# Kernel optimization log

Measured on AMD Instinct MI355X. Metric: run time of the kernel, lower is better.

Reference implementation:

```python
import jax, jax.numpy as jnp
import numpy as np

PF = 16      # PATCH_FEATURES
PFD = 16     # PATCH_FEATURES_DEEP
NCLS = 10

def setup_inputs() -> dict:
    key = jax.random.key(0)
    ks = jax.random.split(key, 7)
    B = 131072
    x = jax.random.normal(ks[0], (B, 1, 28, 28), dtype=jnp.float32)
    # Linear params: W stored as [out, in] like torch, scaled kaiming-uniform-ish
    W1 = jax.random.uniform(ks[1], (PF, 49), jnp.float32, -1, 1) / jnp.sqrt(49.0)
    b1 = jax.random.uniform(ks[2], (PF,), jnp.float32, -1, 1) / jnp.sqrt(49.0)
    W2 = jax.random.uniform(ks[3], (PFD, 4 * PF), jnp.float32, -1, 1) / jnp.sqrt(64.0)
    b2 = jax.random.uniform(ks[4], (PFD,), jnp.float32, -1, 1) / jnp.sqrt(64.0)
    W3 = jax.random.uniform(ks[5], (NCLS, 4 * PFD), jnp.float32, -1, 1) / jnp.sqrt(64.0)
    b3 = jax.random.uniform(ks[6], (NCLS,), jnp.float32, -1, 1) / jnp.sqrt(64.0)
    return {"x": x, "W1": W1, "b1": b1, "W2": W2, "b2": b2, "W3": W3, "b3": b3}


def reference(x, W1, b1, W2, b2, W3, b3):
    # Dropout layers are identity in eval/inference mode.
    B = x.shape[0]
    img = x[:, 0]  # [B,28,28]
    # 16 non-overlapping 7x7 patches, flattened row-major (matches the torch slices)
    p = img.reshape(B, 4, 7, 4, 7).transpose(0, 1, 3, 2, 4).reshape(B, 4, 4, 49)
    # fc1 applied to every patch: one batched GEMM instead of 16 launches
    h = jnp.einsum('bijp,fp->bijf', p, W1) + b1          # [B,4,4,16]
    # group 2x2 patch blocks; concat order (x11,x12,x21,x22) = row-major (ii,jj)
    hb = h.reshape(B, 2, 2, 2, 2, PF).transpose(0, 1, 3, 2, 4, 5).reshape(B, 2, 2, 4 * PF)
    y = jnp.einsum('bijp,fp->bijf', hb, W2) + b2         # [B,2,2,16]
    # concat (y11,y12,y21,y22) row-major over (bi,bj), relu, fc3
    yflat = jax.nn.relu(y).reshape(B, 4 * PFD)           # [B,64]
    z = yflat @ W3.T + b3                                # [B,10]
    return jax.nn.log_softmax(z, axis=1)
```

## Files before the change

### kernel.cpp

```cpp
#include <hip/hip_runtime.h>

typedef float f32x4 __attribute__((ext_vector_type(4)));
typedef short bf16x8 __attribute__((ext_vector_type(8)));

#define XS 464
#define WOFF 29696
#define YOFF 29696
#define YS 144
#define BOFF 38912

__device__ __forceinline__ unsigned short f2bf(float f) {
  unsigned u = __builtin_bit_cast(unsigned, f);
  u += 0x7FFFu + ((u >> 16) & 1u);
  return (unsigned short)(u >> 16);
}
__device__ __forceinline__ unsigned packbf2(float a, float b) {
  return (unsigned)f2bf(a) | ((unsigned)f2bf(b) << 16);
}

__global__ __launch_bounds__(256, 2) void mnist_mfma(
    const float* __restrict__ x, const float* __restrict__ W1,
    const float* __restrict__ b1, const float* __restrict__ W2,
    const float* __restrict__ b2, const float* __restrict__ W3,
    const float* __restrict__ b3, float* __restrict__ out, int nimg)
{
  __shared__ __align__(16) char smem[38976];
  float* smemF = (float*)smem;
  const int tid = threadIdx.x;
  const int lane = tid & 63;
  const int waveid = tid >> 6;

  for (int i = tid; i < 784; i += 256) smemF[i] = W1[i];
  for (int i = tid; i < 1024; i += 256) smemF[784 + i] = W2[i];
  __syncthreads();

  unsigned short* w12b = (unsigned short*)(smem + WOFF);
  for (int e = tid; e < 3136; e += 256) {
    int f2 = e / 196, k = e - f2 * 196;
    int r14 = k / 14, c14 = k - r14 * 14;
    int pp = (r14 % 7) * 7 + (c14 % 7);
    int q = (r14 / 7) * 2 + (c14 / 7);
    float s = 0.f;
#pragma unroll
    for (int f = 0; f < 16; ++f)
      s = fmaf(smemF[f * 49 + pp], smemF[784 + f2 * 64 + q * 16 + f], s);
    w12b[f2 * 232 + k] = f2bf(s);
  }
  for (int e = tid; e < 576; e += 256) {
    int f2 = e / 36;
    w12b[f2 * 232 + 196 + (e - f2 * 36)] = 0;
  }
  if (tid < 16) {
    float s = b2[tid];
#pragma unroll
    for (int k = 0; k < 64; ++k)
      s = fmaf(b1[k & 15], smemF[784 + tid * 64 + k], s);
    smemF[BOFF / 4 + tid] = s;
  }
  __syncthreads();

  bf16x8 wfrag[7];
#pragma unroll
  for (int i = 0; i < 7; ++i)
    wfrag[i] = *(const bf16x8*)(smem + WOFF + (lane & 15) * XS + (lane >> 4) * 16 + 64 * i);

  bf16x8 w3f[2];
  {
    int o = lane & 15, kb = (lane >> 4) * 8;
#pragma unroll
    for (int mi = 0; mi < 2; ++mi) {
      float v[8];
#pragma unroll
      for (int j = 0; j < 8; ++j)
        v[j] = (o < 10) ? W3[o * 64 + kb + 32 * mi + j] : 0.f;
      unsigned t[4];
      t[0] = packbf2(v[0], v[1]); t[1] = packbf2(v[2], v[3]);
      t[2] = packbf2(v[4], v[5]); t[3] = packbf2(v[6], v[7]);
      w3f[mi] = __builtin_bit_cast(bf16x8, *(unsigned(*)[4])t);
    }
  }
  const float b12v = smemF[BOFF / 4 + (lane & 15)];
  float b3v[4];
#pragma unroll
  for (int r = 0; r < 4; ++r) {
    int o = (lane >> 4) * 4 + r;
    b3v[r] = (o < 10) ? b3[o] : 0.f;
  }
  __syncthreads();

  char* xw = smem + waveid * 7424;
#pragma unroll
  for (int j = 0; j < 5; ++j) {
    int idx = lane + 64 * j;
    if (idx < 288) {
      int row = idx / 18, d = idx - row * 18;
      *(unsigned*)(xw + row * XS + 392 + d * 4) = 0;
    }
  }

  unsigned wa0[13]; unsigned strm = 0;
#pragma unroll
  for (int it = 0; it < 13; ++it) {
    int gi = lane + 64 * it;
    int im = gi / 196, rem = gi - im * 196;
    int rr = rem / 7, t = rem - rr * 7;
    int c2 = 2 * t;
    int J = c2 / 7, cq = c2 - 7 * J;
    int row = im * 4 + (rr / 14) * 2 + J;
    int kp = (rr % 14) * 7 + cq;
    wa0[it] = waveid * 7424 + row * XS + kp * 4;
    if (t == 3) strm |= (1u << it);
  }

  const unsigned xrd = waveid * 7424 + (lane & 15) * XS + (lane >> 4) * 16;
  const unsigned yw_base = YOFF + waveid * 2304 + (lane & 15) * 2;
  const unsigned yrd = YOFF + waveid * 2304 + (lane & 15) * YS + (lane >> 4) * 16;

  const int NU = nimg >> 4;
  const int WST = (int)(gridDim.x << 2);
  const int w0 = (int)(blockIdx.x << 2) + waveid;
  const int ng4 = nimg >> 2;

  f32x4 cur[13];
  const f32x4* __restrict__ xq0 = (const f32x4*)x;
  auto issue4 = [&](int g4) {
    const f32x4* p = xq0 + (size_t)g4 * 784;
#pragma unroll
    for (int it = 0; it < 12; ++it) cur[it] = p[lane + 64 * it];
    if (lane < 16) cur[12] = p[768 + lane];
  };

  if (w0 < NU) issue4(w0 * 4);

  for (int u = w0; u < NU; u += WST) {
#pragma unroll 1
    for (int sb = 0; sb < 4; ++sb) {
#pragma unroll
      for (int it = 0; it < 13; ++it) {
        if (it == 12 && lane >= 16) continue;
        f32x4 v = cur[it];
        unsigned a0 = wa0[it];
        unsigned d = ((strm >> it) & 1) ? 440u : 4u;
        *(unsigned*)(smem + a0) = packbf2(v.x, v.y);
        *(unsigned*)(smem + a0 + d) = packbf2(v.z, v.w);
      }
      int ng = (sb < 3) ? (u * 4 + sb + 1) : ((u + WST) * 4);
      if (ng < ng4) issue4(ng);
      f32x4 acc = {0.f, 0.f, 0.f, 0.f};
#pragma unroll
      for (int i = 0; i < 7; ++i) {
        bf16x8 a = *(const bf16x8*)(smem + xrd + 64 * i);
        acc = __builtin_amdgcn_mfma_f32_16x16x32_bf16(a, wfrag[i], acc, 0, 0, 0);
      }
      unsigned yb = yw_base + (unsigned)(sb * 4 + (lane >> 4)) * YS;
#pragma unroll
      for (int r = 0; r < 4; ++r) {
        float yv = fmaxf(acc[r] + b12v, 0.f);
        *(unsigned short*)(smem + yb + r * 32) = f2bf(yv);
      }
    }
    f32x4 z4 = {0.f, 0.f, 0.f, 0.f};
#pragma unroll
    for (int mi = 0; mi < 2; ++mi) {
      bf16x8 bfr = *(const bf16x8*)(smem + yrd + 64 * mi);
      z4 = __builtin_amdgcn_mfma_f32_16x16x32_bf16(w3f[mi], bfr, z4, 0, 0, 0);
    }
    float zv[4], mval = -3.0e38f;
#pragma unroll
    for (int r = 0; r < 4; ++r) {
      zv[r] = z4[r] + b3v[r];
      bool valid = ((lane >> 4) * 4 + r) < 10;
      mval = fmaxf(mval, valid ? zv[r] : -3.0e38f);
    }
    mval = fmaxf(mval, __shfl_xor(mval, 16, 64));
    mval = fmaxf(mval, __shfl_xor(mval, 32, 64));
    float ssum = 0.f;
#pragma unroll
    for (int r = 0; r < 4; ++r) {
      bool valid = ((lane >> 4) * 4 + r) < 10;
      ssum += valid ? __expf(zv[r] - mval) : 0.f;
    }
    ssum += __shfl_xor(ssum, 16, 64);
    ssum += __shfl_xor(ssum, 32, 64);
    const float lse = mval + __logf(ssum);
    float* op = out + (size_t)(u * 16 + (lane & 15)) * 10;
#pragma unroll
    for (int r = 0; r < 4; ++r) {
      int o = (lane >> 4) * 4 + r;
      if (o < 10) op[o] = zv[r] - lse;
    }
  }
}

extern "C" void kernel_launch(void* const* d_in, const int* in_sizes, int n_in,
                              void* d_out, int out_size, void* d_ws, size_t ws_size,
                              hipStream_t stream) {
  const float* x  = (const float*)d_in[0];
  const float* W1 = (const float*)d_in[1];
  const float* b1 = (const float*)d_in[2];
  const float* W2 = (const float*)d_in[3];
  const float* b2 = (const float*)d_in[4];
  const float* W3 = (const float*)d_in[5];
  const float* b3 = (const float*)d_in[6];
  float* out = (float*)d_out;

  const int nimg = in_sizes[0] / 784;
  mnist_mfma<<<1024, 256, 0, stream>>>(x, W1, b1, W2, b2, W3, b3, out, nimg);
}
```

Baseline: 86.53 us.

## Stream input images into LDS via async global_load_lds with double buffering

Replaces the register-staged load, bf16 pack and scatter into a padded LDS tile with direct global-to-LDS DMA of raw fp32 image data into two ping-pong buffers per wave. The A fragments are now gathered and converted to bf16 at MFMA read time, and the fused W1·W2 weight layout is reorganized to match. This is meant to cut VGPR pressure and LDS write traffic and to overlap the next load with compute. The launch shrinks to 512 blocks of 128 threads with much larger LDS per block, which may reduce occupancy and in-flight memory parallelism.

New measurement: 92.51 us. 6.9% more time.

```diff
diff --git a/kernel.cpp b/kernel.cpp
--- a/kernel.cpp
+++ b/kernel.cpp
@@ -1,13 +1,17 @@
 #include <hip/hip_runtime.h>
 
+typedef float f32x2 __attribute__((ext_vector_type(2)));
 typedef float f32x4 __attribute__((ext_vector_type(4)));
 typedef short bf16x8 __attribute__((ext_vector_type(8)));
 
-#define XS 464
-#define WOFF 29696
-#define YOFF 29696
+#define XBUF 12560
+#define XW_STRIDE (2 * XBUF)
+#define XTOT (2 * XW_STRIDE)
+#define W12OFF XTOT
+#define YOFF XTOT
 #define YS 144
-#define BOFF 38912
+#define BOFF (XTOT + 7168)
+#define SMEM_BYTES (BOFF + 64)
 
 __device__ __forceinline__ unsigned short f2bf(float f) {
   unsigned u = __builtin_bit_cast(unsigned, f);
@@ -18,37 +22,45 @@
   return (unsigned)f2bf(a) | ((unsigned)f2bf(b) << 16);
 }
 
-__global__ __launch_bounds__(256, 2) void mnist_mfma(
+__device__ __forceinline__ void dma16(const void* g, void* l) {
+  __builtin_amdgcn_global_load_lds(
+      (const __attribute__((address_space(1))) unsigned*)g,
+      (__attribute__((address_space(3))) unsigned*)l, 16, 0, 0);
+}
+
+__global__ __launch_bounds__(128) void mnist_mfma(
     const float* __restrict__ x, const float* __restrict__ W1,
     const float* __restrict__ b1, const float* __restrict__ W2,
     const float* __restrict__ b2, const float* __restrict__ W3,
     const float* __restrict__ b3, float* __restrict__ out, int nimg)
 {
-  __shared__ __align__(16) char smem[38976];
+  __shared__ __align__(16) char smem[SMEM_BYTES];
   float* smemF = (float*)smem;
   const int tid = threadIdx.x;
   const int lane = tid & 63;
-  const int waveid = tid >> 6;
-
-  for (int i = tid; i < 784; i += 256) smemF[i] = W1[i];
-  for (int i = tid; i < 1024; i += 256) smemF[784 + i] = W2[i];
+  const int wavelocal = tid >> 6;
+
+  if (tid < 16) {
+    int w = tid >> 3, b = (tid >> 2) & 1, d = tid & 3;
+    *(unsigned*)(smem + w * XW_STRIDE + b * XBUF + 12544 + d * 4) = 0;
+  }
+  for (int i = tid; i < 784; i += 128)  smemF[i] = W1[i];
+  for (int i = tid; i < 1024; i += 128) smemF[784 + i] = W2[i];
   __syncthreads();
 
-  unsigned short* w12b = (unsigned short*)(smem + WOFF);
-  for (int e = tid; e < 3136; e += 256) {
-    int f2 = e / 196, k = e - f2 * 196;
-    int r14 = k / 14, c14 = k - r14 * 14;
-    int pp = (r14 % 7) * 7 + (c14 % 7);
-    int q = (r14 / 7) * 2 + (c14 / 7);
+  unsigned short* w12b = (unsigned short*)(smem + W12OFF);
+  for (int e = tid; e < 3584; e += 128) {
+    int f2 = e / 224, k = e - f2 * 224;
+    int rr = k >> 4, cc = k & 15;
     float s = 0.f;
-#pragma unroll
-    for (int f = 0; f < 16; ++f)
-      s = fmaf(smemF[f * 49 + pp], smemF[784 + f2 * 64 + q * 16 + f], s);
-    w12b[f2 * 232 + k] = f2bf(s);
-  }
-  for (int e = tid; e < 576; e += 256) {
-    int f2 = e / 36;
-    w12b[f2 * 232 + 196 + (e - f2 * 36)] = 0;
+    if (cc < 14) {
+      int pp = (rr % 7) * 7 + (cc % 7);
+      int q  = (rr / 7) * 2 + (cc / 7);
+#pragma unroll
+      for (int f = 0; f < 16; ++f)
+        s = fmaf(smemF[f * 49 + pp], smemF[784 + f2 * 64 + q * 16 + f], s);
+    }
+    w12b[f2 * 224 + k] = f2bf(s);
   }
   if (tid < 16) {
     float s = b2[tid];
@@ -62,7 +74,7 @@
   bf16x8 wfrag[7];
 #pragma unroll
   for (int i = 0; i < 7; ++i)
-    wfrag[i] = *(const bf16x8*)(smem + WOFF + (lane & 15) * XS + (lane >> 4) * 16 + 64 * i);
+    wfrag[i] = *(const bf16x8*)(smem + W12OFF + (lane & 15) * 448 + (lane >> 4) * 16 + i * 64);
 
   bf16x8 w3f[2];
   {
@@ -88,106 +100,90 @@
   }
   __syncthreads();
 
-  char* xw = smem + waveid * 7424;
-#pragma unroll
-  for (int j = 0; j < 5; ++j) {
-    int idx = lane + 64 * j;
-    if (idx < 288) {
-      int row = idx / 18, d = idx - row * 18;
-      *(unsigned*)(xw + row * XS + 392 + d * 4) = 0;
-    }
-  }
-
-  unsigned wa0[13]; unsigned strm = 0;
-#pragma unroll
-  for (int it = 0; it < 13; ++it) {
-    int gi = lane + 64 * it;
-    int im = gi / 196, rem = gi - im * 196;
-    int rr = rem / 7, t = rem - rr * 7;
-    int c2 = 2 * t;
-    int J = c2 / 7, cq = c2 - 7 * J;
-    int row = im * 4 + (rr / 14) * 2 + J;
-    int kp = (rr % 14) * 7 + cq;
-    wa0[it] = waveid * 7424 + row * XS + kp * 4;
-    if (t == 3) strm |= (1u << it);
-  }
-
-  const unsigned xrd = waveid * 7424 + (lane & 15) * XS + (lane >> 4) * 16;
-  const unsigned yw_base = YOFF + waveid * 2304 + (lane & 15) * 2;
-  const unsigned yrd = YOFF + waveid * 2304 + (lane & 15) * YS + (lane >> 4) * 16;
+  int abase;
+  {
+    int row = lane & 15, m0 = lane >> 4;
+    int im = row >> 2, q = row & 3, I = q >> 1, J = q & 1;
+    abase = im * 3136 + (I * 14 + (m0 >> 1)) * 112 + J * 56 + (m0 & 1) * 32;
+  }
+  const int XW = wavelocal * XW_STRIDE;
+  const unsigned ywb = YOFF + wavelocal * 2304 + (lane & 15) * 2;
+  const unsigned yrd = YOFF + wavelocal * 2304 + (lane & 15) * YS + (lane >> 4) * 16;
 
   const int NU = nimg >> 4;
-  const int WST = (int)(gridDim.x << 2);
-  const int w0 = (int)(blockIdx.x << 2) + waveid;
-  const int ng4 = nimg >> 2;
-
-  f32x4 cur[13];
-  const f32x4* __restrict__ xq0 = (const f32x4*)x;
-  auto issue4 = [&](int g4) {
-    const f32x4* p = xq0 + (size_t)g4 * 784;
-#pragma unroll
-    for (int it = 0; it < 12; ++it) cur[it] = p[lane + 64 * it];
-    if (lane < 16) cur[12] = p[768 + lane];
+  const int WST = (int)(gridDim.x << 1);
+  const int w0 = (int)(blockIdx.x << 1) + wavelocal;
+  const int nu = (w0 < NU) ? ((NU - w0 + WST - 1) / WST) : 0;
+  const int send = nu * 4;
+
+  auto issue = [&](int s) {
+    int unit = w0 + (s >> 2) * WST;
+    const char* gp = (const char*)x + (size_t)(unit * 4 + (s & 3)) * 12544 + (size_t)(lane * 16);
+    char* lp = smem + XW + (s & 1) * XBUF;
+#pragma unroll
+    for (int it = 0; it < 12; ++it) dma16(gp + it * 1024, lp + it * 1024);
+    if (lane < 16) dma16(gp + 12288, lp + 12288);
   };
 
-  if (w0 < NU) issue4(w0 * 4);
-
-  for (int u = w0; u < NU; u += WST) {
-#pragma unroll 1
-    for (int sb = 0; sb < 4; ++sb) {
-#pragma unroll
-      for (int it = 0; it < 13; ++it) {
-        if (it == 12 && lane >= 16) continue;
-        f32x4 v = cur[it];
-        unsigned a0 = wa0[it];
-        unsigned d = ((strm >> it) & 1) ? 440u : 4u;
-        *(unsigned*)(smem + a0) = packbf2(v.x, v.y);
-        *(unsigned*)(smem + a0 + d) = packbf2(v.z, v.w);
-      }
-      int ng = (sb < 3) ? (u * 4 + sb + 1) : ((u + WST) * 4);
-      if (ng < ng4) issue4(ng);
-      f32x4 acc = {0.f, 0.f, 0.f, 0.f};
-#pragma unroll
-      for (int i = 0; i < 7; ++i) {
-        bf16x8 a = *(const bf16x8*)(smem + xrd + 64 * i);
-        acc = __builtin_amdgcn_mfma_f32_16x16x32_bf16(a, wfrag[i], acc, 0, 0, 0);
-      }
-      unsigned yb = yw_base + (unsigned)(sb * 4 + (lane >> 4)) * YS;
+  if (send > 0) issue(0);
+  if (send > 1) issue(1);
+
+  for (int s = 0; s < send; ++s) {
+    if (s + 1 < send) { asm volatile("s_waitcnt vmcnt(13)" ::: "memory"); }
+    else              { asm volatile("s_waitcnt vmcnt(0)"  ::: "memory"); }
+    __builtin_amdgcn_sched_barrier(0);
+
+    const f32x2* ap = (const f32x2*)(smem + XW + (s & 1) * XBUF + abase);
+    f32x4 acc = {0.f, 0.f, 0.f, 0.f};
+#pragma unroll
+    for (int i = 0; i < 7; ++i) {
+      f32x2 a0 = ap[i * 28], a1 = ap[i * 28 + 1], a2 = ap[i * 28 + 2], a3 = ap[i * 28 + 3];
+      unsigned u[4] = { packbf2(a0.x, a0.y), packbf2(a1.x, a1.y),
+                        packbf2(a2.x, a2.y), packbf2(a3.x, a3.y) };
+      bf16x8 afr = __builtin_bit_cast(bf16x8, *(unsigned(*)[4])u);
+      acc = __builtin_amdgcn_mfma_f32_16x16x32_bf16(afr, wfrag[i], acc, 0, 0, 0);
+    }
+    if (s + 2 < send) issue(s + 2);
+
+    unsigned yb = ywb + (unsigned)((s & 3) * 4 + (lane >> 4)) * YS;
+#pragma unroll
+    for (int r = 0; r < 4; ++r) {
+      float yv = fmaxf(acc[r] + b12v, 0.f);
+      *(unsigned short*)(smem + yb + r * 32) = f2bf(yv);
+    }
+
+    if ((s & 3) == 3) {
+      f32x4 z4 = {0.f, 0.f, 0.f, 0.f};
+#pragma unroll
+      for (int mi = 0; mi < 2; ++mi) {
+        bf16x8 bfr = *(const bf16x8*)(smem + yrd + 64 * mi);
+        z4 = __builtin_amdgcn_mfma_f32_16x16x32_bf16(w3f[mi], bfr, z4, 0, 0, 0);
+      }
+      float zv[4], mval = -3.0e38f;
 #pragma unroll
       for (int r = 0; r < 4; ++r) {
-        float yv = fmaxf(acc[r] + b12v, 0.f);
-        *(unsigned short*)(smem + yb + r * 32) = f2bf(yv);
-      }
-    }
-    f32x4 z4 = {0.f, 0.f, 0.f, 0.f};
-#pragma unroll
-    for (int mi = 0; mi < 2; ++mi) {
-      bf16x8 bfr = *(const bf16x8*)(smem + yrd + 64 * mi);
-      z4 = __builtin_amdgcn_mfma_f32_16x16x32_bf16(w3f[mi], bfr, z4, 0, 0, 0);
-    }
-    float zv[4], mval = -3.0e38f;
-#pragma unroll
-    for (int r = 0; r < 4; ++r) {
-      zv[r] = z4[r] + b3v[r];
-      bool valid = ((lane >> 4) * 4 + r) < 10;
-      mval = fmaxf(mval, valid ? zv[r] : -3.0e38f);
-    }
-    mval = fmaxf(mval, __shfl_xor(mval, 16, 64));
-    mval = fmaxf(mval, __shfl_xor(mval, 32, 64));
-    float ssum = 0.f;
-#pragma unroll
-    for (int r = 0; r < 4; ++r) {
-      bool valid = ((lane >> 4) * 4 + r) < 10;
-      ssum += valid ? __expf(zv[r] - mval) : 0.f;
-    }
-    ssum += __shfl_xor(ssum, 16, 64);
-    ssum += __shfl_xor(ssum, 32, 64);
-    const float lse = mval + __logf(ssum);
-    float* op = out + (size_t)(u * 16 + (lane & 15)) * 10;
-#pragma unroll
-    for (int r = 0; r < 4; ++r) {
-      int o = (lane >> 4) * 4 + r;
-      if (o < 10) op[o] = zv[r] - lse;
+        zv[r] = z4[r] + b3v[r];
+        bool valid = ((lane >> 4) * 4 + r) < 10;
+        mval = fmaxf(mval, valid ? zv[r] : -3.0e38f);
+      }
+      mval = fmaxf(mval, __shfl_xor(mval, 16, 64));
+      mval = fmaxf(mval, __shfl_xor(mval, 32, 64));
+      float ssum = 0.f;
+#pragma unroll
+      for (int r = 0; r < 4; ++r) {
+        bool valid = ((lane >> 4) * 4 + r) < 10;
+        ssum += valid ? __expf(zv[r] - mval) : 0.f;
+      }
+      ssum += __shfl_xor(ssum, 16, 64);
+      ssum += __shfl_xor(ssum, 32, 64);
+      const float lse = mval + __logf(ssum);
+      int unit = w0 + (s >> 2) * WST;
+      float* op = out + (size_t)(unit * 16 + (lane & 15)) * 10;
+#pragma unroll
+      for (int r = 0; r < 4; ++r) {
+        int o = (lane >> 4) * 4 + r;
+        if (o < 10) op[o] = zv[r] - lse;
+      }
     }
   }
 }
@@ -205,5 +201,5 @@
   float* out = (float*)d_out;
 
   const int nimg = in_sizes[0] / 784;
-  mnist_mfma<<<1024, 256, 0, stream>>>(x, W1, b1, W2, b2, W3, b3, out, nimg);
-}
+  mnist_mfma<<<512, 128, 0, stream>>>(x, W1, b1, W2, b2, W3, b3, out, nimg);
+}
```
